# Optimization experiments

Measured on AMD Instinct MI355X. Metric: run time of the kernel, lower is better.

The kernel has to match this reference:

```python
import jax, jax.numpy as jnp
import numpy as np

B, S, D, H = 2, 4096, 1024, 16
DK = D // H


def setup_inputs() -> dict:
    key = jax.random.key(0)
    ks = jax.random.split(key, 7)
    sc = 1.0 / np.sqrt(D)
    return {
        "q": jax.random.normal(ks[0], (B, S, D), jnp.float32),
        "k": jax.random.normal(ks[1], (B, S, D), jnp.float32),
        "v": jax.random.normal(ks[2], (B, S, D), jnp.float32),
        "wq": jax.random.normal(ks[3], (D, D), jnp.float32) * sc,
        "wk": jax.random.normal(ks[4], (D, D), jnp.float32) * sc,
        "wv": jax.random.normal(ks[5], (D, D), jnp.float32) * sc,
        "w0": jax.random.normal(ks[6], (D, D), jnp.float32) * sc,
    }


def reference(q, k, v, wq, wk, wv, w0):
    # Linear(bias=False): y = x @ W^T  (torch convention, W is [out,in])
    qp = jnp.einsum('bsd,ed->bse', q, wq).reshape(B, S, H, DK).transpose(0, 2, 1, 3)
    kp = jnp.einsum('bsd,ed->bse', k, wk).reshape(B, S, H, DK).transpose(0, 2, 1, 3)
    vp = jnp.einsum('bsd,ed->bse', v, wv).reshape(B, S, H, DK).transpose(0, 2, 1, 3)
    scale = 1.0 / jnp.sqrt(jnp.float32(DK))
    att = jnp.einsum('bhqd,bhkd->bhqk', qp, kp) * scale  # [B,H,S,S]
    att = jax.nn.softmax(att, axis=-1)
    x = jnp.einsum('bhqk,bhkd->bhqd', att, vp)  # [B,H,S,DK]
    x = x.transpose(0, 2, 1, 3).reshape(B, S, D)
    out = jnp.einsum('bsd,ed->bse', x, w0)
    return out
```

## Files before the change

kernel.cpp:

```cpp
#include <hip/hip_runtime.h>
#include <hip/hip_bf16.h>
#include <stdint.h>

#define Bb 2
#define Ss 4096
#define Dd 1024
#define Hh 16
#define DKk 64

typedef __attribute__((ext_vector_type(8))) short bf16x8;
typedef __attribute__((ext_vector_type(4))) float f32x4;
typedef __attribute__((ext_vector_type(16))) float f32x16;

#define MFMA16(a, b, c) __builtin_amdgcn_mfma_f32_32x32x16_bf16(a, b, c, 0, 0, 0)

__device__ __forceinline__ unsigned short f2bf(float f) {
    union { float f; unsigned int u; } x; x.f = f;
    return (unsigned short)((x.u + 0x7fffu + ((x.u >> 16) & 1u)) >> 16);
}

__device__ __forceinline__ void gload16(const void* g, void* l) {
    __builtin_amdgcn_global_load_lds(
        (const __attribute__((address_space(1))) void*)g,
        (__attribute__((address_space(3))) void*)l, 16, 0, 0);
}

__device__ __forceinline__ float max3f(float a, float b, float c) {
    return fmaxf(fmaxf(a, b), c);
}

__global__ __launch_bounds__(256) void cvt_all(const float* __restrict__ q, const float* __restrict__ k,
                                               const float* __restrict__ v, const float* __restrict__ wq,
                                               const float* __restrict__ wk, const float* __restrict__ wv,
                                               const float* __restrict__ w0, unsigned short* __restrict__ ws) {
    const int QKV4 = 3 * 2097152;
    const int TOT4 = QKV4 + 4 * 262144;
    int i = blockIdx.x * 256 + threadIdx.x;
    const int stride = gridDim.x * 256;
    ushort4* out = (ushort4*)ws;
    for (; i < TOT4; i += stride) {
        const float4* src;
        int di;
        if (i < QKV4) {
            const int r = i >> 21;
            const float* s = r == 0 ? q : (r == 1 ? k : v);
            src = (const float4*)s + (i & 2097151);
            di = i;
        } else {
            const int j = i - QKV4;
            const int r = j >> 18;
            const float* s = r == 0 ? wq : (r == 1 ? wk : (r == 2 ? wv : w0));
            src = (const float4*)s + (j & 262143);
            di = i + 2097152;
        }
        const float4 vv = *src;
        ushort4 o;
        o.x = f2bf(vv.x); o.y = f2bf(vv.y); o.z = f2bf(vv.z); o.w = f2bf(vv.w);
        out[di] = o;
    }
}

template <int MODE>
__global__ __launch_bounds__(256) void gemm_bt(const unsigned short* __restrict__ A,
                                               const unsigned short* __restrict__ W,
                                               void* __restrict__ Y) {
    __shared__ unsigned short As[128 * 32];
    __shared__ unsigned short Bs[128 * 32];
    const int t = threadIdx.x;
    const int wid = t >> 6, lane = t & 63, q4 = lane >> 4, l16 = lane & 15;
    const int wr = wid >> 1, wc = wid & 1;
    const int arow0 = blockIdx.x * 128;
    const int wrow0 = blockIdx.y * 128;
    f32x4 acc[4][4] = {};
    for (int kt = 0; kt < 1024; kt += 32) {
        __syncthreads();
#pragma unroll
        for (int i = 0; i < 2; i++) {
            const int o = i * 4096 + t * 16;
            const int r = o >> 6, c = (o & 63) >> 1;
            gload16(A + (long)(arow0 + r) * 1024 + kt + c, (char*)As + o);
            gload16(W + (long)(wrow0 + r) * 1024 + kt + c, (char*)Bs + o);
        }
        __syncthreads();
        bf16x8 a[4], b[4];
#pragma unroll
        for (int m = 0; m < 4; m++)
            a[m] = *(const bf16x8*)((const char*)As + (wr * 64 + m * 16 + l16) * 64 + q4 * 16);
#pragma unroll
        for (int n = 0; n < 4; n++)
            b[n] = *(const bf16x8*)((const char*)Bs + (wc * 64 + n * 16 + l16) * 64 + q4 * 16);
#pragma unroll
        for (int m = 0; m < 4; m++)
#pragma unroll
            for (int n = 0; n < 4; n++)
                acc[m][n] = __builtin_amdgcn_mfma_f32_16x16x32_bf16(a[m], b[n], acc[m][n], 0, 0, 0);
    }
    const int rb = arow0 + wr * 64, cb = wrow0 + wc * 64;
#pragma unroll
    for (int m = 0; m < 4; m++)
#pragma unroll
        for (int n = 0; n < 4; n++)
#pragma unroll
            for (int r = 0; r < 4; r++) {
                const int row = rb + m * 16 + q4 * 4 + r;
                const int col = cb + n * 16 + l16;
                const float v = acc[m][n][r];
                if (MODE == 0) {
                    ((unsigned short*)Y)[(long)row * 1024 + col] = f2bf(v);
                } else if (MODE == 1) {
                    const int bb = row >> 12, s = row & 4095;
                    const int hh = col >> 6, dk = col & 63;
                    ((unsigned short*)Y)[(((long)(bb * Hh + hh) * DKk + dk) << 12) + s] = f2bf(v);
                } else {
                    ((float*)Y)[(long)row * 1024 + col] = v;
                }
            }
}

__global__ __launch_bounds__(256, 2) void attn_fwd(const unsigned short* __restrict__ qp,
                                                   const unsigned short* __restrict__ kp,
                                                   const unsigned short* __restrict__ vt,
                                                   unsigned short* __restrict__ xo) {
    __shared__ __align__(16) char smem[32768];
    const int t = threadIdx.x;
    const int wid = t >> 6, lane = t & 63;
    const int l5 = lane & 31;
    const int ihi = lane >> 5;
    const int swz5 = (l5 & 7) ^ ((l5 >> 3) & 3);
    const int qt = blockIdx.x, h = blockIdx.y, b = blockIdx.z;
    const unsigned short* qbase = qp + ((long)b * Ss + qt * 256) * Dd + h * 64;
    const unsigned short* kbase = kp + (long)b * Ss * Dd + h * 64;
    const unsigned short* vbase = vt + (long)(b * Hh + h) * DKk * Ss;

    const int r0 = t >> 3;
    const int s0 = t & 7;
    const int cb0 = s0 ^ (r0 & 7) ^ ((r0 >> 3) & 3);
    const int o0 = t * 16;
    const unsigned short* qsrc = qbase + (long)r0 * Dd + cb0 * 8;
    const unsigned short* ksrc = kbase + (long)r0 * Dd + cb0 * 8;
    const unsigned short* vsrc = vbase + (long)r0 * Ss + cb0 * 8;

#pragma unroll
    for (int i = 0; i < 8; i++)
        gload16(qsrc + (long)i * 32 * Dd, smem + i * 4096 + o0);
    asm volatile("s_waitcnt vmcnt(0)" ::: "memory");
    __builtin_amdgcn_s_barrier();
    asm volatile("" ::: "memory");

    bf16x8 bQ[2][4];
#pragma unroll
    for (int qb = 0; qb < 2; qb++)
#pragma unroll
        for (int m = 0; m < 4; m++) {
            const int chunk = wid * 2 + qb;
            const int slot = (m * 2 + ihi) ^ swz5;
            bQ[qb][m] = *(const bf16x8*)(smem + chunk * 4096 + l5 * 128 + (slot << 4));
        }
    asm volatile("s_waitcnt lgkmcnt(0)" ::: "memory");
    __builtin_amdgcn_s_barrier();
    asm volatile("" ::: "memory");

    gload16(ksrc,                  smem + o0);
    gload16(ksrc + 32 * Dd,        smem + 4096 + o0);
    gload16(vsrc,                  smem + 8192 + o0);
    gload16(vsrc + 32 * Ss,        smem + 12288 + o0);
    gload16(ksrc + 64 * Dd,        smem + 16384 + o0);
    gload16(ksrc + 96 * Dd,        smem + 20480 + o0);
    gload16(vsrc + 64,             smem + 24576 + o0);
    gload16(vsrc + 32 * Ss + 64,   smem + 28672 + o0);
    const unsigned short* pk = ksrc + 128 * Dd;
    const unsigned short* pv = vsrc + 128;
    asm volatile("s_waitcnt vmcnt(4)" ::: "memory");
    __builtin_amdgcn_s_barrier();
    asm volatile("" ::: "memory");

    int adm[4];
#pragma unroll
    for (int m = 0; m < 4; m++)
        adm[m] = l5 * 128 + ((((m * 2 + ihi) ^ swz5)) << 4);

    const float c1f = 0.1803368801111244f;
    float mi[2] = {-1e30f, -1e30f}, li[2] = {0.f, 0.f};
    f32x16 accO[2][2] = {};

    for (int kt2 = 0; kt2 < 64; kt2 += 2) {
#pragma unroll
        for (int hf = 0; hf < 2; hf++) {
            const int kt = kt2 + hf;
            const int BO = hf << 14;
            const char* Kc = smem + BO;
            const char* Vc = smem + BO + 8192;
            f32x16 accS[2][2] = {};
            __builtin_amdgcn_s_setprio(1);
#pragma unroll
            for (int m = 0; m < 4; m++) {
                const bf16x8 aK0 = *(const bf16x8*)(Kc + adm[m]);
                const bf16x8 aK1 = *(const bf16x8*)(Kc + 4096 + adm[m]);
                accS[0][0] = MFMA16(aK0, bQ[0][m], accS[0][0]);
                accS[0][1] = MFMA16(aK1, bQ[0][m], accS[0][1]);
                accS[1][0] = MFMA16(aK0, bQ[1][m], accS[1][0]);
                accS[1][1] = MFMA16(aK1, bQ[1][m], accS[1][1]);
            }
            __builtin_amdgcn_s_setprio(0);
            unsigned pwu[2][2][4][2];
#pragma unroll
            for (int qb = 0; qb < 2; qb++) {
                float m0 = max3f(accS[qb][0][0], accS[qb][0][1], accS[qb][0][2]);
                m0 = max3f(m0, accS[qb][0][3], accS[qb][0][4]);
                m0 = max3f(m0, accS[qb][0][5], accS[qb][0][6]);
                m0 = fmaxf(m0, accS[qb][0][7]);
                float m1 = max3f(accS[qb][0][8], accS[qb][0][9], accS[qb][0][10]);
                m1 = max3f(m1, accS[qb][0][11], accS[qb][0][12]);
                m1 = max3f(m1, accS[qb][0][13], accS[qb][0][14]);
                m1 = fmaxf(m1, accS[qb][0][15]);
                float m2 = max3f(accS[qb][1][0], accS[qb][1][1], accS[qb][1][2]);
                m2 = max3f(m2, accS[qb][1][3], accS[qb][1][4]);
                m2 = max3f(m2, accS[qb][1][5], accS[qb][1][6]);
                m2 = fmaxf(m2, accS[qb][1][7]);
                float m3 = max3f(accS[qb][1][8], accS[qb][1][9], accS[qb][1][10]);
                m3 = max3f(m3, accS[qb][1][11], accS[qb][1][12]);
                m3 = max3f(m3, accS[qb][1][13], accS[qb][1][14]);
                m3 = fmaxf(m3, accS[qb][1][15]);
                const float rmx = fmaxf(max3f(m0, m1, m2), m3);
                if (!__all(rmx * c1f <= mi[qb] + 8.f)) {
                    const float r2 = fmaxf(rmx, __shfl_xor(rmx, 32, 64));
                    const float mn = fmaxf(mi[qb], r2 * c1f);
                    const float alpha = __builtin_amdgcn_exp2f(mi[qb] - mn);
                    mi[qb] = mn;
                    li[qb] *= alpha;
#pragma unroll
                    for (int d = 0; d < 2; d++)
#pragma unroll
                        for (int r = 0; r < 16; r++) accO[d][qb][r] *= alpha;
                }
                float psa[4] = {0.f, 0.f, 0.f, 0.f};
#pragma unroll
                for (int kb = 0; kb < 2; kb++)
#pragma unroll
                    for (int s = 0; s < 4; s++)
#pragma unroll
                        for (int w = 0; w < 2; w++) {
                            const float p0 = __builtin_amdgcn_exp2f(fmaf(accS[qb][kb][4 * s + 2 * w],     c1f, -mi[qb]));
                            const float p1 = __builtin_amdgcn_exp2f(fmaf(accS[qb][kb][4 * s + 2 * w + 1], c1f, -mi[qb]));
                            psa[kb * 2 + w] += p0 + p1;
                            asm("v_cvt_pk_bf16_f32 %0, %1, %2" : "=v"(pwu[qb][kb][s][w]) : "v"(p0), "v"(p1));
                        }
                float ps = (psa[0] + psa[1]) + (psa[2] + psa[3]);
                ps += __shfl_xor(ps, 32, 64);
                li[qb] += ps;
            }
            __builtin_amdgcn_s_setprio(1);
#pragma unroll
            for (int m = 0; m < 4; m++) {
                const bf16x8 aV0 = *(const bf16x8*)(Vc + adm[m]);
                const bf16x8 aV1 = *(const bf16x8*)(Vc + 4096 + adm[m]);
                const int kb = m >> 1, sx = (m & 1) * 2;
#pragma unroll
                for (int qb = 0; qb < 2; qb++) {
                    unsigned x0 = pwu[qb][kb][sx][0], y0 = pwu[qb][kb][sx + 1][0];
                    unsigned x1 = pwu[qb][kb][sx][1], y1 = pwu[qb][kb][sx + 1][1];
                    asm("v_permlane32_swap_b32 %0, %1" : "+v"(x0), "+v"(y0));
                    asm("v_permlane32_swap_b32 %0, %1" : "+v"(x1), "+v"(y1));
                    union { unsigned u[4]; bf16x8 v; } fr;
                    fr.u[0] = x0; fr.u[1] = x1; fr.u[2] = y0; fr.u[3] = y1;
                    accO[0][qb] = MFMA16(aV0, fr.v, accO[0][qb]);
                    accO[1][qb] = MFMA16(aV1, fr.v, accO[1][qb]);
                }
            }
            __builtin_amdgcn_s_setprio(0);
            __builtin_amdgcn_s_barrier();
            asm volatile("" ::: "memory");
            if (kt < 62) {
                char* dst = smem + BO;
                gload16(pk,            dst + o0);
                gload16(pk + 32 * Dd,  dst + 4096 + o0);
                gload16(pv,            dst + 8192 + o0);
                gload16(pv + 32 * Ss,  dst + 12288 + o0);
                pk += 64 * Dd;
                pv += 64;
                asm volatile("s_waitcnt vmcnt(4)" ::: "memory");
            } else {
                asm volatile("s_waitcnt vmcnt(0)" ::: "memory");
            }
            __builtin_amdgcn_s_barrier();
            asm volatile("" ::: "memory");
        }
    }

#pragma unroll
    for (int qb = 0; qb < 2; qb++) {
        const float rli = 1.0f / li[qb];
        const int chunk = wid * 2 + qb;
#pragma unroll
        for (int dblk = 0; dblk < 2; dblk++)
#pragma unroll
            for (int tt = 0; tt < 8; tt++) {
                const unsigned short b0 = f2bf(accO[dblk][qb][2 * tt] * rli);
                const unsigned short b1 = f2bf(accO[dblk][qb][2 * tt + 1] * rli);
                const int slot = (dblk * 4 + (tt >> 1)) ^ swz5;
                const int phys = chunk * 4096 + l5 * 128 + (slot << 4) + ihi * 8 + (tt & 1) * 4;
                *(unsigned*)(smem + phys) = ((unsigned)b1 << 16) | b0;
            }
    }
    __syncthreads();
#pragma unroll
    for (int p = 0; p < 8; p++) {
        const uint4 val = *(const uint4*)(smem + p * 4096 + o0);
        const long row = (long)qt * 256 + p * 32 + r0;
        *(uint4*)(xo + ((long)b * Ss + row) * Dd + h * 64 + cb0 * 8) = val;
    }
}

extern "C" void kernel_launch(void* const* d_in, const int* in_sizes, int n_in,
                              void* d_out, int out_size, void* d_ws, size_t ws_size,
                              hipStream_t stream) {
    const float* q  = (const float*)d_in[0];
    const float* k  = (const float*)d_in[1];
    const float* v  = (const float*)d_in[2];
    const float* wq = (const float*)d_in[3];
    const float* wk = (const float*)d_in[4];
    const float* wv = (const float*)d_in[5];
    const float* w0 = (const float*)d_in[6];

    unsigned short* ws = (unsigned short*)d_ws;
    const long NE = (long)Bb * Ss * Dd;
    unsigned short* qb  = ws;
    unsigned short* kb  = ws + NE;
    unsigned short* vb  = ws + 2 * NE;
    unsigned short* x1  = ws + 3 * NE;
    unsigned short* wqb = ws + 4 * NE;
    unsigned short* wkb = wqb + 1048576;
    unsigned short* wvb = wkb + 1048576;
    unsigned short* w0b = wvb + 1048576;

    cvt_all<<<2048, 256, 0, stream>>>(q, k, v, wq, wk, wv, w0, ws);

    dim3 gg(64, 8);
    gemm_bt<0><<<gg, 256, 0, stream>>>(qb, wqb, x1);
    gemm_bt<0><<<gg, 256, 0, stream>>>(kb, wkb, qb);
    gemm_bt<1><<<gg, 256, 0, stream>>>(vb, wvb, kb);
    dim3 ga(16, 16, 2);
    attn_fwd<<<ga, 256, 0, stream>>>(x1, qb, kb, vb);
    gemm_bt<2><<<gg, 256, 0, stream>>>(vb, w0b, (float*)d_out);
}
```

Baseline: 285.2 us.

## Prescale Q projection and compute softmax row sums with an MFMA

The softmax scale times log2(e) is folded into the Q projection GEMM through a new output mode, which removes the per-element FMA in the attention exponent. Row sums of P are no longer accumulated by VALU adds plus a cross-lane shuffle. They come from an extra MFMA against a ones-like A operand. Exponentiation and bf16 packing also move into the PV loop to shorten the live range of the P registers. The cost is more MFMA work per tile, extra accumulator registers, and the Q projection rounded to bf16 after scaling.

Measured after the change: 275.2 us. -3.5%, faster.

```diff
diff --git a/kernel.cpp b/kernel.cpp
--- a/kernel.cpp
+++ b/kernel.cpp
@@ -111,6 +111,8 @@
                     const int bb = row >> 12, s = row & 4095;
                     const int hh = col >> 6, dk = col & 63;
                     ((unsigned short*)Y)[(((long)(bb * Hh + hh) * DKk + dk) << 12) + s] = f2bf(v);
+                } else if (MODE == 3) {
+                    ((unsigned short*)Y)[(long)row * 1024 + col] = f2bf(v * 0.1803368801111244f);
                 } else {
                     ((float*)Y)[(long)row * 1024 + col] = v;
                 }
@@ -179,9 +181,15 @@
     for (int m = 0; m < 4; m++)
         adm[m] = l5 * 128 + ((((m * 2 + ihi) ^ swz5)) << 4);
 
-    const float c1f = 0.1803368801111244f;
-    float mi[2] = {-1e30f, -1e30f}, li[2] = {0.f, 0.f};
+    union { unsigned u[4]; bf16x8 v; } onesA;
+    {
+        const unsigned ov = (l5 == 0) ? 0x3F803F80u : 0u;
+        onesA.u[0] = ov; onesA.u[1] = ov; onesA.u[2] = ov; onesA.u[3] = ov;
+    }
+
+    float mi[2] = {-1e30f, -1e30f};
     f32x16 accO[2][2] = {};
+    f32x16 accP[2] = {};
 
     for (int kt2 = 0; kt2 < 64; kt2 += 2) {
 #pragma unroll
@@ -202,7 +210,6 @@
                 accS[1][1] = MFMA16(aK1, bQ[1][m], accS[1][1]);
             }
             __builtin_amdgcn_s_setprio(0);
-            unsigned pwu[2][2][4][2];
 #pragma unroll
             for (int qb = 0; qb < 2; qb++) {
                 float m0 = max3f(accS[qb][0][0], accS[qb][0][1], accS[qb][0][2]);
@@ -222,32 +229,17 @@
                 m3 = max3f(m3, accS[qb][1][13], accS[qb][1][14]);
                 m3 = fmaxf(m3, accS[qb][1][15]);
                 const float rmx = fmaxf(max3f(m0, m1, m2), m3);
-                if (!__all(rmx * c1f <= mi[qb] + 8.f)) {
+                if (!__all(rmx <= mi[qb] + 8.f)) {
                     const float r2 = fmaxf(rmx, __shfl_xor(rmx, 32, 64));
-                    const float mn = fmaxf(mi[qb], r2 * c1f);
+                    const float mn = fmaxf(mi[qb], r2);
                     const float alpha = __builtin_amdgcn_exp2f(mi[qb] - mn);
                     mi[qb] = mn;
-                    li[qb] *= alpha;
+                    accP[qb][0] *= alpha;
 #pragma unroll
                     for (int d = 0; d < 2; d++)
 #pragma unroll
                         for (int r = 0; r < 16; r++) accO[d][qb][r] *= alpha;
                 }
-                float psa[4] = {0.f, 0.f, 0.f, 0.f};
-#pragma unroll
-                for (int kb = 0; kb < 2; kb++)
-#pragma unroll
-                    for (int s = 0; s < 4; s++)
-#pragma unroll
-                        for (int w = 0; w < 2; w++) {
-                            const float p0 = __builtin_amdgcn_exp2f(fmaf(accS[qb][kb][4 * s + 2 * w],     c1f, -mi[qb]));
-                            const float p1 = __builtin_amdgcn_exp2f(fmaf(accS[qb][kb][4 * s + 2 * w + 1], c1f, -mi[qb]));
-                            psa[kb * 2 + w] += p0 + p1;
-                            asm("v_cvt_pk_bf16_f32 %0, %1, %2" : "=v"(pwu[qb][kb][s][w]) : "v"(p0), "v"(p1));
-                        }
-                float ps = (psa[0] + psa[1]) + (psa[2] + psa[3]);
-                ps += __shfl_xor(ps, 32, 64);
-                li[qb] += ps;
             }
             __builtin_amdgcn_s_setprio(1);
 #pragma unroll
@@ -257,14 +249,29 @@
                 const int kb = m >> 1, sx = (m & 1) * 2;
 #pragma unroll
                 for (int qb = 0; qb < 2; qb++) {
-                    unsigned x0 = pwu[qb][kb][sx][0], y0 = pwu[qb][kb][sx + 1][0];
-                    unsigned x1 = pwu[qb][kb][sx][1], y1 = pwu[qb][kb][sx + 1][1];
-                    asm("v_permlane32_swap_b32 %0, %1" : "+v"(x0), "+v"(y0));
-                    asm("v_permlane32_swap_b32 %0, %1" : "+v"(x1), "+v"(y1));
+                    const float miq = mi[qb];
+                    unsigned w00, w01, w10, w11;
+                    {
+                        const float a0 = __builtin_amdgcn_exp2f(accS[qb][kb][4 * sx + 0] - miq);
+                        const float a1 = __builtin_amdgcn_exp2f(accS[qb][kb][4 * sx + 1] - miq);
+                        const float a2 = __builtin_amdgcn_exp2f(accS[qb][kb][4 * sx + 2] - miq);
+                        const float a3 = __builtin_amdgcn_exp2f(accS[qb][kb][4 * sx + 3] - miq);
+                        const float b0 = __builtin_amdgcn_exp2f(accS[qb][kb][4 * sx + 4] - miq);
+                        const float b1 = __builtin_amdgcn_exp2f(accS[qb][kb][4 * sx + 5] - miq);
+                        const float b2 = __builtin_amdgcn_exp2f(accS[qb][kb][4 * sx + 6] - miq);
+                        const float b3 = __builtin_amdgcn_exp2f(accS[qb][kb][4 * sx + 7] - miq);
+                        asm("v_cvt_pk_bf16_f32 %0, %1, %2" : "=v"(w00) : "v"(a0), "v"(a1));
+                        asm("v_cvt_pk_bf16_f32 %0, %1, %2" : "=v"(w01) : "v"(a2), "v"(a3));
+                        asm("v_cvt_pk_bf16_f32 %0, %1, %2" : "=v"(w10) : "v"(b0), "v"(b1));
+                        asm("v_cvt_pk_bf16_f32 %0, %1, %2" : "=v"(w11) : "v"(b2), "v"(b3));
+                    }
+                    asm("v_permlane32_swap_b32 %0, %1" : "+v"(w00), "+v"(w10));
+                    asm("v_permlane32_swap_b32 %0, %1" : "+v"(w01), "+v"(w11));
                     union { unsigned u[4]; bf16x8 v; } fr;
-                    fr.u[0] = x0; fr.u[1] = x1; fr.u[2] = y0; fr.u[3] = y1;
+                    fr.u[0] = w00; fr.u[1] = w01; fr.u[2] = w10; fr.u[3] = w11;
                     accO[0][qb] = MFMA16(aV0, fr.v, accO[0][qb]);
                     accO[1][qb] = MFMA16(aV1, fr.v, accO[1][qb]);
+                    accP[qb]    = MFMA16(onesA.v, fr.v, accP[qb]);
                 }
             }
             __builtin_amdgcn_s_setprio(0);
@@ -289,7 +296,8 @@
 
 #pragma unroll
     for (int qb = 0; qb < 2; qb++) {
-        const float rli = 1.0f / li[qb];
+        const float liq = __shfl(accP[qb][0], l5, 64);
+        const float rli = 1.0f / liq;
         const int chunk = wid * 2 + qb;
 #pragma unroll
         for (int dblk = 0; dblk < 2; dblk++)
@@ -336,7 +344,7 @@
     cvt_all<<<2048, 256, 0, stream>>>(q, k, v, wq, wk, wv, w0, ws);
 
     dim3 gg(64, 8);
-    gemm_bt<0><<<gg, 256, 0, stream>>>(qb, wqb, x1);
+    gemm_bt<3><<<gg, 256, 0, stream>>>(qb, wqb, x1);
     gemm_bt<0><<<gg, 256, 0, stream>>>(kb, wkb, qb);
     gemm_bt<1><<<gg, 256, 0, stream>>>(vb, wvb, kb);
     dim3 ga(16, 16, 2);
```
